# Optimization experiments

Measured on AMD Instinct MI355X. Metric: run time of the kernel, lower is better.

Reference implementation:

```python
import jax, jax.numpy as jnp
import numpy as np
from jax import lax


def _conv3x3(x, w, b):
    # x: [b,C,H,W], w: [Cout,Cin,3,3] (OIHW), same padding, stride 1
    y = lax.conv_general_dilated(
        x, w, window_strides=(1, 1), padding='SAME',
        dimension_numbers=('NCHW', 'OIHW', 'NCHW'))
    return y + b[None, :, None, None]


def setup_inputs() -> dict:
    key = jax.random.key(0)
    ks = jax.random.split(key, 8)
    b, C, H, W = 8, 256, 64, 64
    wscale = 0.02  # keep conv outputs O(1) so softmax logits are well-conditioned
    X = jax.random.normal(ks[0], (b, C, H, W), dtype=jnp.float32)
    w1 = jax.random.normal(ks[1], (C, C, 3, 3), dtype=jnp.float32) * wscale
    b1 = jax.random.normal(ks[2], (C,), dtype=jnp.float32) * 0.01
    w2 = jax.random.normal(ks[3], (C, C, 3, 3), dtype=jnp.float32) * wscale
    b2 = jax.random.normal(ks[4], (C,), dtype=jnp.float32) * 0.01
    w3 = jax.random.normal(ks[5], (C, C, 3, 3), dtype=jnp.float32) * wscale
    b3 = jax.random.normal(ks[6], (C,), dtype=jnp.float32) * 0.01
    # alpha_init=0 in the original makes the output identically zero; use a
    # small nonzero alpha so fwd/bwd are non-degenerate for correctness checks.
    alpha = jax.random.normal(ks[7], (), dtype=jnp.float32)
    return {"X": X, "w1": w1, "b1": b1, "w2": w2, "b2": b2,
            "w3": w3, "b3": b3, "alpha": alpha}


def reference(X, w1, b1, w2, b2, w3, b3, alpha):
    b, C, H, W = X.shape
    N = H * W
    A = _conv3x3(X, w1, b1).reshape(b, C, N)  # [b,C,N]
    B = _conv3x3(X, w2, b2).reshape(b, C, N)  # [b,C,N]
    D = _conv3x3(X, w3, b3).reshape(b, C, N)  # [b,C,N]
    # M = softmax(A^T B) over last dim; M: [b,N,N]
    M = jnp.einsum('bcn,bcm->bnm', A, B)
    M = jax.nn.softmax(M, axis=-1)
    # weighted_C = M @ D^T -> [b,N,C]; then to [b,C,H,W]
    out = jnp.einsum('bnm,bcm->bcn', M, D).reshape(b, C, H, W)
    return alpha * out
```

## Files before the change

kernel.cpp:

```cpp
#include <hip/hip_runtime.h>
#include <math.h>

#define BATCH 8
#define CCH   256
#define HH    64
#define WW    64
#define NN    4096

#define BNC   (BATCH * NN * CCH)
#define WELEMS (3 * 8 * 9 * 256 * 32)

typedef __bf16   bf16x8 __attribute__((ext_vector_type(8)));
typedef _Float16 f16x8  __attribute__((ext_vector_type(8)));
typedef _Float16 f16x4  __attribute__((ext_vector_type(4)));
typedef float    f32x4  __attribute__((ext_vector_type(4)));

__global__ void wtrans_kernel(const float* __restrict__ w1,
                              const float* __restrict__ w2,
                              const float* __restrict__ w3,
                              _Float16* __restrict__ Whi,
                              _Float16* __restrict__ Wlo) {
    int e = blockIdx.x * 256 + threadIdx.x;
    int t = e;
    const int ci  = t & 31;  t >>= 5;
    const int co  = t & 255; t >>= 8;
    const int tap = t % 9;   t /= 9;
    const int cc  = t & 7;   t >>= 3;
    const int conv = t;
    const float* src = (conv == 0) ? w1 : (conv == 1) ? w2 : w3;
    const float v = src[co * 2304 + (cc * 32 + ci) * 9 + tap];
    const _Float16 h = (_Float16)v;
    Whi[e] = h;
    Wlo[e] = (_Float16)(v - (float)h);
}

__global__ __launch_bounds__(256)
void xsplit_kernel(const float* __restrict__ X,
                   _Float16* __restrict__ Xhi, _Float16* __restrict__ Xlo) {
    __shared__ float T[64][65];
    const int h = blockIdx.x, c0 = blockIdx.y * 64, bb = blockIdx.z;
    const int t = threadIdx.x;
    const int row = t >> 2, q = (t & 3) * 16;
#pragma unroll
    for (int k = 0; k < 4; ++k) {
        float4 v = *(const float4*)&X[(((size_t)bb * CCH + c0 + row) * HH + h) * WW + q + k * 4];
        *(float4*)&T[row][q + k * 4] = v;
    }
    __syncthreads();
    f16x8 h0, h1, l0, l1;
#pragma unroll
    for (int j = 0; j < 8; ++j) {
        float v = T[q + j][row];
        _Float16 hh = (_Float16)v;
        h0[j] = hh; l0[j] = (_Float16)(v - (float)hh);
    }
#pragma unroll
    for (int j = 0; j < 8; ++j) {
        float v = T[q + 8 + j][row];
        _Float16 hh = (_Float16)v;
        h1[j] = hh; l1[j] = (_Float16)(v - (float)hh);
    }
    const size_t g = (((size_t)bb * HH + h) * WW + row) * CCH + c0 + q;
    *(f16x8*)(Xhi + g) = h0;  *(f16x8*)(Xhi + g + 8) = h1;
    *(f16x8*)(Xlo + g) = l0;  *(f16x8*)(Xlo + g + 8) = l1;
}

__global__ __launch_bounds__(512, 2)
void conv_mfma_kernel(const _Float16* __restrict__ Xhi, const _Float16* __restrict__ Xlo,
                      const _Float16* __restrict__ Whi, const _Float16* __restrict__ Wlo,
                      const float* __restrict__ b1, const float* __restrict__ b2,
                      const float* __restrict__ b3,
                      __bf16* __restrict__ Qhi, __bf16* __restrict__ Qlo,
                      __bf16* __restrict__ Khi, __bf16* __restrict__ Klo,
                      float* __restrict__ Dws) {
    const int h0   = blockIdx.x * 2;
    const int bb   = blockIdx.y;
    const int conv = blockIdx.z;
    const int tid  = threadIdx.x;
    const int wave = tid >> 6;
    const int lane = tid & 63;
    const int quad = lane >> 4;
    const int l16  = lane & 15;
    const int mg   = wave >> 2;
    const int ng   = wave & 3;

    __shared__ _Float16 XsH[4 * 66 * 32];
    __shared__ _Float16 XsL[4 * 66 * 32];

    const bool threePass = (conv < 2);
    const float* bias = (conv == 0) ? b1 : (conv == 1) ? b2 : b3;

    f32x4 acc[4][4];
#pragma unroll
    for (int j = 0; j < 4; ++j) {
        const float bv = bias[ng * 64 + j * 16 + l16];
#pragma unroll
        for (int i = 0; i < 4; ++i) acc[i][j] = (f32x4){bv, bv, bv, bv};
    }

    const f16x8 zf = {0, 0, 0, 0, 0, 0, 0, 0};
    const int xrow = tid >> 7;
    const int xw   = (tid >> 1) & 63;
    const int xch  = (tid & 1) * 16;
    const int xc0  = (tid & 1) * 2;

    if (tid < 256) {
        const int zr = tid >> 6, zc = ((tid >> 5) & 1) ? 65 : 0, zch = tid & 31;
        XsH[(zr * 66 + zc) * 32 + zch] = (_Float16)0;
        XsL[(zr * 66 + zc) * 32 + zch] = (_Float16)0;
    }

    int xb[3];
#pragma unroll
    for (int dw = 0; dw < 3; ++dw)
        xb[dw] = mg * 2112 + (l16 + dw) * 32 + ((quad ^ ((l16 + dw) & 3)) * 8);

    const int wloff = (ng * 64 + l16) * 32 + quad * 8;
    const _Float16* WhB = Whi + (size_t)conv * 589824;
    const _Float16* WlB = Wlo + (size_t)conv * 589824;

    f16x8 wbh[2][4], wbl[2][4];
#pragma unroll
    for (int j = 0; j < 4; ++j) {
        wbh[0][j] = *(const f16x8*)(WhB + wloff + j * 512);
        wbl[0][j] = zf;
        if (threePass) wbl[0][j] = *(const f16x8*)(WlB + wloff + j * 512);
    }

    for (int cc2 = 0; cc2 < 4; ++cc2) {
#pragma unroll
        for (int ccp = 0; ccp < 2; ++ccp) {
            const int cc = cc2 * 2 + ccp;
            __syncthreads();
            {
                const int h = h0 - 1 + xrow;
                f16x8 a0 = zf, a1 = zf, b0 = zf, b1v = zf;
                if ((unsigned)h < (unsigned)HH) {
                    const size_t g = (((size_t)bb * HH + h) * WW + xw) * CCH + cc * 32 + xch;
                    a0 = *(const f16x8*)(Xhi + g);  a1 = *(const f16x8*)(Xhi + g + 8);
                    if (threePass) { b0 = *(const f16x8*)(Xlo + g);  b1v = *(const f16x8*)(Xlo + g + 8); }
                }
                const int col = xw + 1;
                const int lbase = (xrow * 66 + col) * 32;
                const int s3 = col & 3;
                *(f16x8*)&XsH[lbase + ((xc0 ^ s3) * 8)]       = a0;
                *(f16x8*)&XsH[lbase + (((xc0 + 1) ^ s3) * 8)] = a1;
                if (threePass) {
                    *(f16x8*)&XsL[lbase + ((xc0 ^ s3) * 8)]       = b0;
                    *(f16x8*)&XsL[lbase + (((xc0 + 1) ^ s3) * 8)] = b1v;
                }
            }
            __syncthreads();

#pragma unroll
            for (int tap = 0; tap < 9; ++tap) {
                const int p  = (ccp + tap) & 1;
                const int np = p ^ 1;
                {
                    const int nst = cc * 9 + tap + 1;
                    const size_t nb = (size_t)(nst == 72 ? 0 : nst) * 8192 + wloff;
#pragma unroll
                    for (int j = 0; j < 4; ++j) {
                        wbh[np][j] = *(const f16x8*)(WhB + nb + j * 512);
                        if (threePass) wbl[np][j] = *(const f16x8*)(WlB + nb + j * 512);
                    }
                }
                const int dh = tap / 3, dw = tap % 3;
                f16x8 ah[4], al[4];
#pragma unroll
                for (int i = 0; i < 4; ++i) {
                    const int off = xb[dw] + dh * 2112 + i * 512;
                    ah[i] = *(const f16x8*)&XsH[off];
                    if (threePass) al[i] = *(const f16x8*)&XsL[off];
                }
#pragma unroll
                for (int j = 0; j < 4; ++j) {
                    if (threePass) {
#pragma unroll
                        for (int i = 0; i < 4; ++i) {
                            acc[i][j] = __builtin_amdgcn_mfma_f32_16x16x32_f16(ah[i], wbh[p][j], acc[i][j], 0, 0, 0);
                            acc[i][j] = __builtin_amdgcn_mfma_f32_16x16x32_f16(al[i], wbh[p][j], acc[i][j], 0, 0, 0);
                            acc[i][j] = __builtin_amdgcn_mfma_f32_16x16x32_f16(ah[i], wbl[p][j], acc[i][j], 0, 0, 0);
                        }
                    } else {
#pragma unroll
                        for (int i = 0; i < 4; ++i)
                            acc[i][j] = __builtin_amdgcn_mfma_f32_16x16x32_f16(ah[i], wbh[p][j], acc[i][j], 0, 0, 0);
                    }
                }
            }
        }
    }

    const size_t nb = (size_t)bb * NN + (size_t)(h0 + mg) * 64;
    if (threePass) {
        __bf16* Hi = conv ? Khi : Qhi;
        __bf16* Lo = conv ? Klo : Qlo;
#pragma unroll
        for (int i = 0; i < 4; ++i) {
            const int wx0 = i * 16 + quad * 4;
#pragma unroll
            for (int j = 0; j < 4; ++j) {
                const int co = ng * 64 + j * 16 + l16;
#pragma unroll
                for (int r = 0; r < 4; ++r) {
                    const float v = acc[i][j][r];
                    const size_t idx = (nb + wx0 + r) * CCH + co;
                    const __bf16 hq = (__bf16)v;
                    Hi[idx] = hq;
                    Lo[idx] = (__bf16)(v - (float)hq);
                }
            }
        }
    } else {
#pragma unroll
        for (int i = 0; i < 4; ++i) {
            const int wx0 = i * 16 + quad * 4;
#pragma unroll
            for (int j = 0; j < 4; ++j) {
                const int co = ng * 64 + j * 16 + l16;
#pragma unroll
                for (int r = 0; r < 4; ++r)
                    Dws[(nb + wx0 + r) * CCH + co] = acc[i][j][r];
            }
        }
    }
}

__global__ __launch_bounds__(256)
void transpose_v_kernel(const float* __restrict__ D, _Float16* __restrict__ Vt) {
    __shared__ float T[64][65];
    const int n0 = blockIdx.x * 64, c0 = blockIdx.y * 64, bb = blockIdx.z;
    const int t = threadIdx.x;
    const int row = t >> 2, q = (t & 3) * 16;
#pragma unroll
    for (int k = 0; k < 4; ++k) {
        float4 v = *(const float4*)(D + ((size_t)bb * NN + n0 + row) * CCH + c0 + q + k * 4);
        *(float4*)&T[row][q + k * 4] = v;
    }
    __syncthreads();
    f16x8 o0, o1;
#pragma unroll
    for (int j = 0; j < 8; ++j) o0[j] = (_Float16)T[q + j][row];
#pragma unroll
    for (int j = 0; j < 8; ++j) o1[j] = (_Float16)T[q + 8 + j][row];
    _Float16* dst = Vt + ((size_t)bb * CCH + c0 + row) * NN + n0 + q;
    *(f16x8*)dst = o0;
    *(f16x8*)(dst + 8) = o1;
}

__global__ __launch_bounds__(512, 2)
void attn_mfma_kernel(const __bf16* __restrict__ Qhi, const __bf16* __restrict__ Qlo,
                      const __bf16* __restrict__ Khi, const __bf16* __restrict__ Klo,
                      const _Float16* __restrict__ Vt, const float* __restrict__ alpha_p,
                      float* __restrict__ out) {
    const int bb = blockIdx.x & 7;
    const int qb = blockIdx.x >> 3;
    const int n0 = qb * 128;
    const int tid  = threadIdx.x;
    const int wave = tid >> 6;
    const int lane = tid & 63;
    const int quad = lane >> 4;
    const int l16  = lane & 15;
    const int xq   = l16 & 7;

    extern __shared__ __align__(16) unsigned char smem[];
    _Float16* PwA  = (_Float16*)(smem + 98304);
    float*    Ssc  = (float*)(smem + 133120);
    float*    Linv = (float*)(smem + 133632);
    _Float16* Pw   = PwA + wave * (16 * 136);

    bf16x8 qh[8], ql[8];
    {
        const size_t base = ((size_t)bb * NN + n0 + wave * 16 + l16) * CCH + quad * 8;
#pragma unroll
        for (int ks = 0; ks < 8; ++ks) {
            qh[ks] = *(const bf16x8*)(Qhi + base + ks * 32);
            ql[ks] = *(const bf16x8*)(Qlo + base + ks * 32);
        }
    }

    f32x4 Oacc[2][8];
#pragma unroll
    for (int cf = 0; cf < 2; ++cf)
#pragma unroll
        for (int qt = 0; qt < 8; ++qt) Oacc[cf][qt] = (f32x4){0.f, 0.f, 0.f, 0.f};
    float m_i = -INFINITY, l_i = 0.f;

    const int krow = tid >> 2, kq4 = tid & 3;

    bf16x8 kph[2], kpl[2];

    auto kload = [&](int m0_, int cc_) {
#pragma unroll
        for (int i = 0; i < 2; ++i) {
            const int u = kq4 * 2 + i;
            const size_t g = ((size_t)bb * NN + m0_ + krow) * CCH + cc_ * 64 + u * 8;
            kph[i] = *(const bf16x8*)(Khi + g);
            kpl[i] = *(const bf16x8*)(Klo + g);
        }
    };
    auto kwrite = [&](unsigned char* base) {
        __bf16* H = (__bf16*)base;
        __bf16* L = (__bf16*)(base + 16384);
#pragma unroll
        for (int i = 0; i < 2; ++i) {
            const int u = kq4 * 2 + i;
            const int lo = krow * 64 + ((u ^ (krow & 7)) * 8);
            *(bf16x8*)&H[lo] = kph[i];
            *(bf16x8*)&L[lo] = kpl[i];
        }
    };

    f32x4 Sacc[8];
    auto schunk = [&](int cc, const unsigned char* base) {
        const __bf16* KH = (const __bf16*)base;
        const __bf16* KL = (const __bf16*)(base + 16384);
#pragma unroll
        for (int ks = 0; ks < 2; ++ks) {
            const int kq = cc * 2 + ks;
#pragma unroll
            for (int kvt = 0; kvt < 8; ++kvt) {
                const int off = (kvt * 16 + l16) * 64 + (((ks * 4 + quad) ^ xq) * 8);
                const bf16x8 kh = *(const bf16x8*)&KH[off];
                const bf16x8 kl = *(const bf16x8*)&KL[off];
                Sacc[kvt] = __builtin_amdgcn_mfma_f32_16x16x32_bf16(kh, qh[kq], Sacc[kvt], 0, 0, 0);
                Sacc[kvt] = __builtin_amdgcn_mfma_f32_16x16x32_bf16(kl, qh[kq], Sacc[kvt], 0, 0, 0);
                Sacc[kvt] = __builtin_amdgcn_mfma_f32_16x16x32_bf16(kh, ql[kq], Sacc[kvt], 0, 0, 0);
            }
        }
    };

    kload(0, 0);
    kwrite(smem);
    kload(0, 1);
    kwrite(smem + 32768);
    __syncthreads();

    int rot = 0;

    for (int t = 0; t < 32; ++t) {
        const int m0 = t * 128;
        const int m0n = (t == 31) ? 0 : m0 + 128;
        unsigned char* P0 = smem + rot * 32768;
        unsigned char* P1 = smem + ((rot + 1) % 3) * 32768;
        unsigned char* F  = smem + ((rot + 2) % 3) * 32768;

#pragma unroll
        for (int kvt = 0; kvt < 8; ++kvt) Sacc[kvt] = (f32x4){0.f, 0.f, 0.f, 0.f};

        kload(m0, 2);
        schunk(0, P0);
        kwrite(F);
        kload(m0, 3);
        schunk(1, P1);
        __syncthreads();
        kwrite(P0);
        schunk(2, F);
        __syncthreads();
        schunk(3, P0);

        f16x8 vf[2][4];
#pragma unroll
        for (int cf = 0; cf < 2; ++cf)
#pragma unroll
            for (int kvf = 0; kvf < 4; ++kvf)
                vf[cf][kvf] = *(const f16x8*)(Vt +
                    ((size_t)bb * CCH + wave * 32 + cf * 16 + l16) * NN +
                    m0 + kvf * 32 + quad * 8);

        float mx = -INFINITY;
#pragma unroll
        for (int kvt = 0; kvt < 8; ++kvt)
#pragma unroll
            for (int r = 0; r < 4; ++r) mx = fmaxf(mx, Sacc[kvt][r]);
        mx = fmaxf(mx, __shfl_xor(mx, 16, 64));
        mx = fmaxf(mx, __shfl_xor(mx, 32, 64));
        const float mnew = fmaxf(m_i, mx);
        float rs = 0.f;
#pragma unroll
        for (int kvt = 0; kvt < 8; ++kvt) {
            f16x4 pw;
#pragma unroll
            for (int r = 0; r < 4; ++r) {
                const float p = __expf(Sacc[kvt][r] - mnew);
                rs += p;
                pw[r] = (_Float16)p;
            }
            *(f16x4*)&Pw[l16 * 136 + kvt * 16 + quad * 4] = pw;
        }
        rs += __shfl_xor(rs, 16, 64);
        rs += __shfl_xor(rs, 32, 64);
        const float scale = __expf(m_i - mnew);
        if (quad == 0) Ssc[wave * 16 + l16] = scale;
        l_i = l_i * scale + rs;
        m_i = mnew;
        __syncthreads();

        float sc[8];
#pragma unroll
        for (int qt = 0; qt < 8; ++qt) sc[qt] = Ssc[qt * 16 + l16];
#pragma unroll
        for (int cf = 0; cf < 2; ++cf)
#pragma unroll
            for (int qt = 0; qt < 8; ++qt) {
                Oacc[cf][qt][0] *= sc[qt];
                Oacc[cf][qt][1] *= sc[qt];
                Oacc[cf][qt][2] *= sc[qt];
                Oacc[cf][qt][3] *= sc[qt];
            }

        kload(m0n, 0);
#pragma unroll
        for (int qt = 0; qt < 4; ++qt) {
            const _Float16* Pq = PwA + qt * (16 * 136);
            f16x8 pf[4];
#pragma unroll
            for (int kvf = 0; kvf < 4; ++kvf)
                pf[kvf] = *(const f16x8*)&Pq[l16 * 136 + kvf * 32 + quad * 8];
#pragma unroll
            for (int cf = 0; cf < 2; ++cf)
#pragma unroll
                for (int kvf = 0; kvf < 4; ++kvf)
                    Oacc[cf][qt] = __builtin_amdgcn_mfma_f32_16x16x32_f16(vf[cf][kvf], pf[kvf], Oacc[cf][qt], 0, 0, 0);
        }
        kwrite(P1);
        kload(m0n, 1);
#pragma unroll
        for (int qt = 4; qt < 8; ++qt) {
            const _Float16* Pq = PwA + qt * (16 * 136);
            f16x8 pf[4];
#pragma unroll
            for (int kvf = 0; kvf < 4; ++kvf)
                pf[kvf] = *(const f16x8*)&Pq[l16 * 136 + kvf * 32 + quad * 8];
#pragma unroll
            for (int cf = 0; cf < 2; ++cf)
#pragma unroll
                for (int kvf = 0; kvf < 4; ++kvf)
                    Oacc[cf][qt] = __builtin_amdgcn_mfma_f32_16x16x32_f16(vf[cf][kvf], pf[kvf], Oacc[cf][qt], 0, 0, 0);
        }
        kwrite(F);
        __syncthreads();

        rot = (rot + 1) == 3 ? 0 : rot + 1;
    }

    const float alpha = *alpha_p;
    if (quad == 0) Linv[wave * 16 + l16] = alpha / l_i;
    __syncthreads();
#pragma unroll
    for (int qt = 0; qt < 8; ++qt) {
        const float inv = Linv[qt * 16 + l16];
#pragma unroll
        for (int cf = 0; cf < 2; ++cf)
#pragma unroll
            for (int r = 0; r < 4; ++r) {
                const int c = wave * 32 + cf * 16 + quad * 4 + r;
                out[((size_t)bb * CCH + c) * NN + n0 + qt * 16 + l16] = Oacc[cf][qt][r] * inv;
            }
    }
}

extern "C" void kernel_launch(void* const* d_in, const int* in_sizes, int n_in,
                              void* d_out, int out_size, void* d_ws, size_t ws_size,
                              hipStream_t stream) {
    const float* X  = (const float*)d_in[0];
    const float* w1 = (const float*)d_in[1];
    const float* b1 = (const float*)d_in[2];
    const float* w2 = (const float*)d_in[3];
    const float* b2 = (const float*)d_in[4];
    const float* w3 = (const float*)d_in[5];
    const float* b3 = (const float*)d_in[6];
    const float* alpha = (const float*)d_in[7];
    float* out = (float*)d_out;

    float*    Dws = (float*)d_ws;
    __bf16*   Qhi = (__bf16*)(Dws + (size_t)BNC);
    __bf16*   Qlo = Qhi + (size_t)BNC;
    __bf16*   Khi = Qlo + (size_t)BNC;
    __bf16*   Klo = Khi + (size_t)BNC;
    _Float16* Vt  = (_Float16*)(Klo + (size_t)BNC);
    _Float16* Xhi = Vt + (size_t)BNC;
    _Float16* Xlo = Xhi + (size_t)BNC;
    _Float16* Whi = Xlo + (size_t)BNC;
    _Float16* Wlo = Whi + (size_t)WELEMS;

    wtrans_kernel<<<dim3(WELEMS / 256), 256, 0, stream>>>(w1, w2, w3, Whi, Wlo);

    xsplit_kernel<<<dim3(HH, CCH / 64, BATCH), 256, 0, stream>>>(X, Xhi, Xlo);

    conv_mfma_kernel<<<dim3(HH / 2, BATCH, 3), 512, 0, stream>>>(
        Xhi, Xlo, Whi, Wlo, b1, b2, b3, Qhi, Qlo, Khi, Klo, Dws);

    transpose_v_kernel<<<dim3(NN / 64, CCH / 64, BATCH), 256, 0, stream>>>(Dws, Vt);

    attn_mfma_kernel<<<dim3(256), 512, 134144, stream>>>(
        Qhi, Qlo, Khi, Klo, Vt, alpha, out);
}
```

Before: 559.6 us.

## Double-buffer conv input tiles and stream K tiles via global_load_lds

The conv kernel now double-buffers its shared-memory input tile. The next channel chunk is loaded into registers during the first taps and written to the alternate buffer mid-loop, which removes one barrier per chunk and hides the global-load latency. The attention kernel replaces its register-staged K hi/lo loads with direct global-to-LDS async loads and reorders when K chunks are issued. It also drops the barrier at the end of each iteration, adding one barrier only before the epilogue. This cuts VGPR pressure and LDS write instructions, but relies on the reordered barriers still protecting the rotating buffers and doubles the conv kernel's LDS use.

Result: slower. 608.4 us (+8.7%).

```diff
diff --git a/kernel.cpp b/kernel.cpp
--- a/kernel.cpp
+++ b/kernel.cpp
@@ -14,6 +14,9 @@
 typedef _Float16 f16x8  __attribute__((ext_vector_type(8)));
 typedef _Float16 f16x4  __attribute__((ext_vector_type(4)));
 typedef float    f32x4  __attribute__((ext_vector_type(4)));
+
+typedef const __attribute__((address_space(1))) unsigned int* gu32p;
+typedef __attribute__((address_space(3))) unsigned int* lu32p;
 
 __global__ void wtrans_kernel(const float* __restrict__ w1,
                               const float* __restrict__ w2,
@@ -84,8 +87,9 @@
     const int mg   = wave >> 2;
     const int ng   = wave & 3;
 
-    __shared__ _Float16 XsH[4 * 66 * 32];
-    __shared__ _Float16 XsL[4 * 66 * 32];
+    __shared__ _Float16 XsH[2 * 4 * 66 * 32];
+    __shared__ _Float16 XsL[2 * 4 * 66 * 32];
+    const int XB = 4 * 66 * 32;
 
     const bool threePass = (conv < 2);
     const float* bias = (conv == 0) ? b1 : (conv == 1) ? b2 : b3;
@@ -104,16 +108,42 @@
     const int xch  = (tid & 1) * 16;
     const int xc0  = (tid & 1) * 2;
 
-    if (tid < 256) {
-        const int zr = tid >> 6, zc = ((tid >> 5) & 1) ? 65 : 0, zch = tid & 31;
-        XsH[(zr * 66 + zc) * 32 + zch] = (_Float16)0;
-        XsL[(zr * 66 + zc) * 32 + zch] = (_Float16)0;
+    {
+        const int zb = tid >> 8, zr = (tid >> 6) & 3;
+        const int zc = ((tid >> 5) & 1) ? 65 : 0, zch = tid & 31;
+        const int o = zb * XB + (zr * 66 + zc) * 32 + zch;
+        XsH[o] = (_Float16)0;
+        XsL[o] = (_Float16)0;
     }
 
     int xb[3];
 #pragma unroll
     for (int dw = 0; dw < 3; ++dw)
         xb[dw] = mg * 2112 + (l16 + dw) * 32 + ((quad ^ ((l16 + dw) & 3)) * 8);
+
+    const int scol  = xw + 1;
+    const int slb   = (xrow * 66 + scol) * 32;
+    const int ss3   = scol & 3;
+
+    auto xload = [&](int cc, f16x8& a0, f16x8& a1, f16x8& b0, f16x8& b1v) {
+        const int h = h0 - 1 + xrow;
+        a0 = zf; a1 = zf; b0 = zf; b1v = zf;
+        if ((unsigned)h < (unsigned)HH) {
+            const size_t g = (((size_t)bb * HH + h) * WW + xw) * CCH + cc * 32 + xch;
+            a0 = *(const f16x8*)(Xhi + g);  a1 = *(const f16x8*)(Xhi + g + 8);
+            if (threePass) { b0 = *(const f16x8*)(Xlo + g);  b1v = *(const f16x8*)(Xlo + g + 8); }
+        }
+    };
+    auto xwrite = [&](int buf, const f16x8& a0, const f16x8& a1,
+                      const f16x8& b0, const f16x8& b1v) {
+        const int lb = buf * XB + slb;
+        *(f16x8*)&XsH[lb + ((xc0 ^ ss3) * 8)]       = a0;
+        *(f16x8*)&XsH[lb + (((xc0 + 1) ^ ss3) * 8)] = a1;
+        if (threePass) {
+            *(f16x8*)&XsL[lb + ((xc0 ^ ss3) * 8)]       = b0;
+            *(f16x8*)&XsL[lb + (((xc0 + 1) ^ ss3) * 8)] = b1v;
+        }
+    };
 
     const int wloff = (ng * 64 + l16) * 32 + quad * 8;
     const _Float16* WhB = Whi + (size_t)conv * 589824;
@@ -127,38 +157,31 @@
         if (threePass) wbl[0][j] = *(const f16x8*)(WlB + wloff + j * 512);
     }
 
+    {
+        f16x8 a0, a1, b0, b1v;
+        xload(0, a0, a1, b0, b1v);
+        xwrite(0, a0, a1, b0, b1v);
+    }
+    __syncthreads();
+
     for (int cc2 = 0; cc2 < 4; ++cc2) {
 #pragma unroll
         for (int ccp = 0; ccp < 2; ++ccp) {
             const int cc = cc2 * 2 + ccp;
-            __syncthreads();
-            {
-                const int h = h0 - 1 + xrow;
-                f16x8 a0 = zf, a1 = zf, b0 = zf, b1v = zf;
-                if ((unsigned)h < (unsigned)HH) {
-                    const size_t g = (((size_t)bb * HH + h) * WW + xw) * CCH + cc * 32 + xch;
-                    a0 = *(const f16x8*)(Xhi + g);  a1 = *(const f16x8*)(Xhi + g + 8);
-                    if (threePass) { b0 = *(const f16x8*)(Xlo + g);  b1v = *(const f16x8*)(Xlo + g + 8); }
-                }
-                const int col = xw + 1;
-                const int lbase = (xrow * 66 + col) * 32;
-                const int s3 = col & 3;
-                *(f16x8*)&XsH[lbase + ((xc0 ^ s3) * 8)]       = a0;
-                *(f16x8*)&XsH[lbase + (((xc0 + 1) ^ s3) * 8)] = a1;
-                if (threePass) {
-                    *(f16x8*)&XsL[lbase + ((xc0 ^ s3) * 8)]       = b0;
-                    *(f16x8*)&XsL[lbase + (((xc0 + 1) ^ s3) * 8)] = b1v;
-                }
-            }
-            __syncthreads();
-
-#pragma unroll
-            for (int tap = 0; tap < 9; ++tap) {
+            const int rbase = ccp * XB;
+            const int ccW = cc * 73728;
+
+            f16x8 sa0, sa1, sb0, sb1;
+            const bool doStage = (cc < 7);
+            if (doStage) xload(cc + 1, sa0, sa1, sb0, sb1);
+
+#pragma unroll
+            for (int tap = 0; tap < 4; ++tap) {
                 const int p  = (ccp + tap) & 1;
                 const int np = p ^ 1;
                 {
                     const int nst = cc * 9 + tap + 1;
-                    const size_t nb = (size_t)(nst == 72 ? 0 : nst) * 8192 + wloff;
+                    const size_t nb = (size_t)nst * 8192 + wloff;
 #pragma unroll
                     for (int j = 0; j < 4; ++j) {
                         wbh[np][j] = *(const f16x8*)(WhB + nb + j * 512);
@@ -169,7 +192,7 @@
                 f16x8 ah[4], al[4];
 #pragma unroll
                 for (int i = 0; i < 4; ++i) {
-                    const int off = xb[dw] + dh * 2112 + i * 512;
+                    const int off = rbase + xb[dw] + dh * 2112 + i * 512;
                     ah[i] = *(const f16x8*)&XsH[off];
                     if (threePass) al[i] = *(const f16x8*)&XsL[off];
                 }
@@ -189,6 +212,48 @@
                     }
                 }
             }
+
+            if (doStage) xwrite(ccp ^ 1, sa0, sa1, sb0, sb1);
+
+#pragma unroll
+            for (int tap = 4; tap < 9; ++tap) {
+                const int p  = (ccp + tap) & 1;
+                const int np = p ^ 1;
+                {
+                    const int nst = cc * 9 + tap + 1;
+                    const size_t nb = (size_t)(nst == 72 ? 0 : nst) * 8192 + wloff;
+#pragma unroll
+                    for (int j = 0; j < 4; ++j) {
+                        wbh[np][j] = *(const f16x8*)(WhB + nb + j * 512);
+                        if (threePass) wbl[np][j] = *(const f16x8*)(WlB + nb + j * 512);
+                    }
+                }
+                const int dh = tap / 3, dw = tap % 3;
+                f16x8 ah[4], al[4];
+#pragma unroll
+                for (int i = 0; i < 4; ++i) {
+                    const int off = rbase + xb[dw] + dh * 2112 + i * 512;
+                    ah[i] = *(const f16x8*)&XsH[off];
+                    if (threePass) al[i] = *(const f16x8*)&XsL[off];
+                }
+#pragma unroll
+                for (int j = 0; j < 4; ++j) {
+                    if (threePass) {
+#pragma unroll
+                        for (int i = 0; i < 4; ++i) {
+                            acc[i][j] = __builtin_amdgcn_mfma_f32_16x16x32_f16(ah[i], wbh[p][j], acc[i][j], 0, 0, 0);
+                            acc[i][j] = __builtin_amdgcn_mfma_f32_16x16x32_f16(al[i], wbh[p][j], acc[i][j], 0, 0, 0);
+                            acc[i][j] = __builtin_amdgcn_mfma_f32_16x16x32_f16(ah[i], wbl[p][j], acc[i][j], 0, 0, 0);
+                        }
+                    } else {
+#pragma unroll
+                        for (int i = 0; i < 4; ++i)
+                            acc[i][j] = __builtin_amdgcn_mfma_f32_16x16x32_f16(ah[i], wbh[p][j], acc[i][j], 0, 0, 0);
+                    }
+                }
+            }
+
+            __syncthreads();
         }
     }
 
@@ -287,28 +352,17 @@
         for (int qt = 0; qt < 8; ++qt) Oacc[cf][qt] = (f32x4){0.f, 0.f, 0.f, 0.f};
     float m_i = -INFINITY, l_i = 0.f;
 
-    const int krow = tid >> 2, kq4 = tid & 3;
-
-    bf16x8 kph[2], kpl[2];
-
-    auto kload = [&](int m0_, int cc_) {
+    const int grow = lane >> 3;
+    const int gu   = (lane & 7) ^ grow;
+    auto kgll = [&](int m0_, int cc_, unsigned char* dst) {
 #pragma unroll
         for (int i = 0; i < 2; ++i) {
-            const int u = kq4 * 2 + i;
-            const size_t g = ((size_t)bb * NN + m0_ + krow) * CCH + cc_ * 64 + u * 8;
-            kph[i] = *(const bf16x8*)(Khi + g);
-            kpl[i] = *(const bf16x8*)(Klo + g);
-        }
-    };
-    auto kwrite = [&](unsigned char* base) {
-        __bf16* H = (__bf16*)base;
-        __bf16* L = (__bf16*)(base + 16384);
-#pragma unroll
-        for (int i = 0; i < 2; ++i) {
-            const int u = kq4 * 2 + i;
-            const int lo = krow * 64 + ((u ^ (krow & 7)) * 8);
-            *(bf16x8*)&H[lo] = kph[i];
-            *(bf16x8*)&L[lo] = kpl[i];
+            const int row = wave * 16 + i * 8 + grow;
+            const size_t g = ((size_t)bb * NN + m0_ + row) * CCH + cc_ * 64 + gu * 8;
+            __builtin_amdgcn_global_load_lds(
+                (gu32p)(Khi + g), (lu32p)(dst + wave * 2048 + i * 1024), 16, 0, 0);
+            __builtin_amdgcn_global_load_lds(
+                (gu32p)(Klo + g), (lu32p)(dst + 16384 + wave * 2048 + i * 1024), 16, 0, 0);
         }
     };
 
@@ -331,10 +385,8 @@
         }
     };
 
-    kload(0, 0);
-    kwrite(smem);
-    kload(0, 1);
-    kwrite(smem + 32768);
+    kgll(0, 0, smem);
+    kgll(0, 1, smem + 32768);
     __syncthreads();
 
     int rot = 0;
@@ -349,15 +401,15 @@
 #pragma unroll
         for (int kvt = 0; kvt < 8; ++kvt) Sacc[kvt] = (f32x4){0.f, 0.f, 0.f, 0.f};
 
-        kload(m0, 2);
+        kgll(m0, 2, F);
         schunk(0, P0);
-        kwrite(F);
-        kload(m0, 3);
         schunk(1, P1);
         __syncthreads();
-        kwrite(P0);
+        kgll(m0, 3, P0);
+        kgll(m0n, 0, P1);
         schunk(2, F);
         __syncthreads();
+        kgll(m0n, 1, F);
         schunk(3, P0);
 
         f16x8 vf[2][4];
@@ -410,9 +462,8 @@
                 Oacc[cf][qt][3] *= sc[qt];
             }
 
-        kload(m0n, 0);
-#pragma unroll
-        for (int qt = 0; qt < 4; ++qt) {
+#pragma unroll
+        for (int qt = 0; qt < 8; ++qt) {
             const _Float16* Pq = PwA + qt * (16 * 136);
             f16x8 pf[4];
 #pragma unroll
@@ -424,28 +475,12 @@
                 for (int kvf = 0; kvf < 4; ++kvf)
                     Oacc[cf][qt] = __builtin_amdgcn_mfma_f32_16x16x32_f16(vf[cf][kvf], pf[kvf], Oacc[cf][qt], 0, 0, 0);
         }
-        kwrite(P1);
-        kload(m0n, 1);
-#pragma unroll
-        for (int qt = 4; qt < 8; ++qt) {
-            const _Float16* Pq = PwA + qt * (16 * 136);
-            f16x8 pf[4];
-#pragma unroll
-            for (int kvf = 0; kvf < 4; ++kvf)
-                pf[kvf] = *(const f16x8*)&Pq[l16 * 136 + kvf * 32 + quad * 8];
-#pragma unroll
-            for (int cf = 0; cf < 2; ++cf)
-#pragma unroll
-                for (int kvf = 0; kvf < 4; ++kvf)
-                    Oacc[cf][qt] = __builtin_amdgcn_mfma_f32_16x16x32_f16(vf[cf][kvf], pf[kvf], Oacc[cf][qt], 0, 0, 0);
-        }
-        kwrite(F);
-        __syncthreads();
 
         rot = (rot + 1) == 3 ? 0 : rot + 1;
     }
 
     const float alpha = *alpha_p;
+    __syncthreads();
     if (quad == 0) Linv[wave * 16 + l16] = alpha / l_i;
     __syncthreads();
 #pragma unroll
```
